# Kernel tuning notes

Measured on AMD Instinct MI355X. Metric: run time of the kernel, lower is better.

Reference implementation:

```python
import jax, jax.numpy as jnp
import numpy as np

B, C_IN, H, W = 4, 128, 32, 32
C_SKIP, C_OUT = 64, 64
D_MODEL = 2 * C_SKIP            # 128 (channels after concat)
D_STATE, D_CONV, EXPAND = 16, 4, 2
D_INNER = EXPAND * D_MODEL      # 256
DT_RANK = int(np.ceil(D_MODEL / 16))  # 8
LN_EPS = 1e-5


def setup_inputs() -> dict:
    key = jax.random.key(0)
    ks = jax.random.split(key, 12)
    s = 0.02
    return {
        "x": jax.random.normal(ks[0], (B, C_IN, H, W), jnp.float32),
        "skip_x": jax.random.normal(ks[1], (B, C_SKIP, 2 * H, 2 * W), jnp.float32),
        # ConvTranspose2d(in, skip, k=2, s=2): torch weight layout (in, out, kh, kw)
        "up_w": jax.random.normal(ks[2], (C_IN, C_SKIP, 2, 2), jnp.float32) * s,
        "up_b": jnp.zeros((C_SKIP,), jnp.float32),
        # Mamba params (torch Linear layout: (out_features, in_features))
        "in_proj_w": jax.random.normal(ks[3], (2 * D_INNER, D_MODEL), jnp.float32) * s,
        "conv1d_w": jax.random.normal(ks[4], (D_INNER, 1, D_CONV), jnp.float32) * s,
        "conv1d_b": jnp.zeros((D_INNER,), jnp.float32),
        "x_proj_w": jax.random.normal(ks[5], (DT_RANK + 2 * D_STATE, D_INNER), jnp.float32) * s,
        "dt_proj_w": jax.random.normal(ks[6], (D_INNER, DT_RANK), jnp.float32) * s,
        "dt_proj_b": jnp.zeros((D_INNER,), jnp.float32),
        "A_log": jnp.log(jnp.broadcast_to(jnp.arange(1, D_STATE + 1, dtype=jnp.float32), (D_INNER, D_STATE))),
        "Dp": jnp.ones((D_INNER,), jnp.float32),
        "out_proj_w": jax.random.normal(ks[7], (D_MODEL, D_INNER), jnp.float32) * s,
        "ln_gamma": jnp.ones((D_MODEL,), jnp.float32),
        "ln_beta": jnp.zeros((D_MODEL,), jnp.float32),
        # Conv2d 1x1 (out, in)
        "convout_w": jax.random.normal(ks[8], (C_OUT, D_MODEL), jnp.float32) * s,
        "convout_b": jnp.zeros((C_OUT,), jnp.float32),
    }


def _selective_scan(u, delta, A, Bm, Cm, Dp):
    # u, delta: (B,L,Din); A: (Din,Ds); Bm, Cm: (B,L,Ds)
    deltaA = jnp.exp(delta[..., None] * A)                        # (B,L,Din,Ds)
    deltaBu = delta[..., None] * Bm[:, :, None, :] * u[..., None]  # (B,L,Din,Ds)

    def step(h, xs):
        dA, dBu, c = xs                 # (B,Din,Ds),(B,Din,Ds),(B,Ds)
        h = dA * h + dBu
        y = jnp.einsum('bdn,bn->bd', h, c)
        return h, y

    h0 = jnp.zeros((u.shape[0], D_INNER, D_STATE), u.dtype)
    xs = (deltaA.transpose(1, 0, 2, 3), deltaBu.transpose(1, 0, 2, 3), Cm.transpose(1, 0, 2))
    _, ys = jax.lax.scan(step, h0, xs)  # (L,B,Din)
    return ys.transpose(1, 0, 2) + u * Dp


def _mamba(seq, in_proj_w, conv1d_w, conv1d_b, x_proj_w, dt_proj_w, dt_proj_b, A_log, Dp, out_proj_w):
    # seq: (B, L, D_MODEL)
    xz = seq @ in_proj_w.T                      # (B,L,2*Din)
    u, z = jnp.split(xz, 2, axis=-1)
    # depthwise causal conv1d along L
    uc = u.transpose(0, 2, 1)                   # (B,Din,L)
    uc = jax.lax.conv_general_dilated(
        uc, conv1d_w, window_strides=(1,), padding=[(D_CONV - 1, 0)],
        feature_group_count=D_INNER, dimension_numbers=('NCH', 'OIH', 'NCH'))
    uc = uc + conv1d_b[None, :, None]
    u = jax.nn.silu(uc.transpose(0, 2, 1))      # (B,L,Din)
    dbc = u @ x_proj_w.T                        # (B,L,DT_RANK+2*Ds)
    dt, Bm, Cm = jnp.split(dbc, [DT_RANK, DT_RANK + D_STATE], axis=-1)
    delta = jax.nn.softplus(dt @ dt_proj_w.T + dt_proj_b)
    A = -jnp.exp(A_log)
    y = _selective_scan(u, delta, A, Bm, Cm, Dp)
    y = y * jax.nn.silu(z)
    return y @ out_proj_w.T                     # (B,L,D_MODEL)


def reference(x, skip_x, up_w, up_b, in_proj_w, conv1d_w, conv1d_b, x_proj_w,
              dt_proj_w, dt_proj_b, A_log, Dp, out_proj_w, ln_gamma, ln_beta,
              convout_w, convout_b):
    b, _, h, w = x.shape
    # ConvTranspose2d k=2 s=2: each pixel expands to a 2x2 block
    up = jnp.einsum('bchw,coij->bohiwj', x, up_w).reshape(b, C_SKIP, 2 * h, 2 * w)
    up = up + up_b[None, :, None, None]
    xc = jnp.concatenate([up, skip_x], axis=1)  # (B, D_MODEL, 2H, 2W)
    Hh, Ww = xc.shape[2], xc.shape[3]
    seq = xc.reshape(b, D_MODEL, Hh * Ww).transpose(0, 2, 1)  # (B,L,D)
    y = _mamba(seq, in_proj_w, conv1d_w, conv1d_b, x_proj_w, dt_proj_w,
               dt_proj_b, A_log, Dp, out_proj_w)
    xm = y.transpose(0, 2, 1).reshape(b, D_MODEL, Hh, Ww)
    # permute -> LayerNorm over channels -> permute back
    xn = xm.transpose(0, 2, 3, 1)
    mu = xn.mean(-1, keepdims=True)
    var = xn.var(-1, keepdims=True)
    xn = (xn - mu) * jax.lax.rsqrt(var + LN_EPS) * ln_gamma + ln_beta
    xm = jax.nn.silu(xn.transpose(0, 3, 1, 2))
    out = jnp.einsum('bchw,oc->bohw', xm, convout_w) + convout_b[None, :, None, None]
    return out
```

## Files before the change

### kernel.cpp

```cpp
#include <hip/hip_runtime.h>

#define L_SEQ 4096
#define DM 128
#define DIN 256
#define NC 128
#define CHUNK 32

__global__ __launch_bounds__(256) void upcat_kernel(
    const float* __restrict__ x, const float* __restrict__ skip,
    const float* __restrict__ up_w, const float* __restrict__ up_b,
    float* __restrict__ seq) {
  int b = blockIdx.x >> 6, hh = blockIdx.x & 63;
  int h = hh >> 1, i = hh & 1;
  int tid = threadIdx.x;
  __shared__ float xs[128][32];
  __shared__ float wsh[2][128][64];
  for (int e = tid; e < 1024; e += 256) {
    int c = e >> 3, q = e & 7;
    *(float4*)&xs[c][q * 4] =
        *(const float4*)(x + (((size_t)b * 128 + c) * 32 + h) * 32 + q * 4);
  }
  for (int e = tid; e < 8192; e += 256) {
    int c = e >> 6, o = e & 63;
    float2 v = *(const float2*)(up_w + c * 256 + o * 4 + i * 2);
    wsh[0][c][o] = v.x;
    wsh[1][c][o] = v.y;
  }
  __syncthreads();
  int tx = tid & 15, ty = tid >> 4;
  float4 bv = *(const float4*)(up_b + tx * 4);
  float acc[4][4];
#pragma unroll
  for (int a = 0; a < 4; ++a) {
    acc[a][0] = bv.x; acc[a][1] = bv.y; acc[a][2] = bv.z; acc[a][3] = bv.w;
  }
#pragma unroll 4
  for (int c = 0; c < 128; ++c) {
    float x0 = xs[c][ty * 2];
    float x1 = xs[c][ty * 2 + 1];
    float4 w0 = *(const float4*)&wsh[0][c][tx * 4];
    float4 w1 = *(const float4*)&wsh[1][c][tx * 4];
    acc[0][0] = fmaf(x0, w0.x, acc[0][0]); acc[0][1] = fmaf(x0, w0.y, acc[0][1]);
    acc[0][2] = fmaf(x0, w0.z, acc[0][2]); acc[0][3] = fmaf(x0, w0.w, acc[0][3]);
    acc[1][0] = fmaf(x0, w1.x, acc[1][0]); acc[1][1] = fmaf(x0, w1.y, acc[1][1]);
    acc[1][2] = fmaf(x0, w1.z, acc[1][2]); acc[1][3] = fmaf(x0, w1.w, acc[1][3]);
    acc[2][0] = fmaf(x1, w0.x, acc[2][0]); acc[2][1] = fmaf(x1, w0.y, acc[2][1]);
    acc[2][2] = fmaf(x1, w0.z, acc[2][2]); acc[2][3] = fmaf(x1, w0.w, acc[2][3]);
    acc[3][0] = fmaf(x1, w1.x, acc[3][0]); acc[3][1] = fmaf(x1, w1.y, acc[3][1]);
    acc[3][2] = fmaf(x1, w1.z, acc[3][2]); acc[3][3] = fmaf(x1, w1.w, acc[3][3]);
  }
  size_t mrow_base = (size_t)b * L_SEQ + (size_t)hh * 64;
#pragma unroll
  for (int a = 0; a < 4; ++a) {
    int ww = ty * 4 + a;
    *(float4*)(seq + (mrow_base + ww) * DM + tx * 4) =
        make_float4(acc[a][0], acc[a][1], acc[a][2], acc[a][3]);
  }
  for (int e = tid; e < 4096; e += 256) {
    int c = e & 63, ww = e >> 6;
    seq[(mrow_base + ww) * DM + 64 + c] =
        skip[((size_t)b * 64 + c) * (size_t)L_SEQ + hh * 64 + ww];
  }
}

__global__ __launch_bounds__(256) void gemm_bt128(
    const float* __restrict__ A, const float* __restrict__ W,
    float* __restrict__ C, int M, int N, int K) {
  __shared__ float As[32][132];
  __shared__ float Ws[32][68];
  int m0 = blockIdx.x * 128, n0 = blockIdx.y * 64;
  int tid = threadIdx.x;
  int tx = tid & 15, ty = tid >> 4;
  float acc[8][4];
#pragma unroll
  for (int a = 0; a < 8; ++a)
#pragma unroll
    for (int bb = 0; bb < 4; ++bb) acc[a][bb] = 0.f;

  for (int k0 = 0; k0 < K; k0 += 32) {
    __syncthreads();
    for (int e = tid; e < 1024; e += 256) {
      int r = e >> 3, c4 = (e & 7) << 2;
      float4 va = *(const float4*)(A + (size_t)(m0 + r) * K + k0 + c4);
      As[c4 + 0][r] = va.x; As[c4 + 1][r] = va.y;
      As[c4 + 2][r] = va.z; As[c4 + 3][r] = va.w;
    }
    for (int e = tid; e < 512; e += 256) {
      int r = e >> 3, c4 = (e & 7) << 2;
      float4 vw = *(const float4*)(W + (size_t)(n0 + r) * K + k0 + c4);
      Ws[c4 + 0][r] = vw.x; Ws[c4 + 1][r] = vw.y;
      Ws[c4 + 2][r] = vw.z; Ws[c4 + 3][r] = vw.w;
    }
    __syncthreads();
#pragma unroll
    for (int kk = 0; kk < 32; ++kk) {
      float4 a0 = *(const float4*)(&As[kk][ty * 8]);
      float4 a1 = *(const float4*)(&As[kk][ty * 8 + 4]);
      float4 wv = *(const float4*)(&Ws[kk][tx * 4]);
      float a_[8] = {a0.x, a0.y, a0.z, a0.w, a1.x, a1.y, a1.z, a1.w};
      float w_[4] = {wv.x, wv.y, wv.z, wv.w};
#pragma unroll
      for (int a = 0; a < 8; ++a)
#pragma unroll
        for (int bb = 0; bb < 4; ++bb)
          acc[a][bb] = fmaf(a_[a], w_[bb], acc[a][bb]);
    }
  }
#pragma unroll
  for (int a = 0; a < 8; ++a)
#pragma unroll
    for (int bb = 0; bb < 4; ++bb)
      C[(size_t)(m0 + ty * 8 + a) * N + n0 + tx * 4 + bb] = acc[a][bb];
}

__global__ __launch_bounds__(256) void gemm_bt(
    const float* __restrict__ A, const float* __restrict__ W,
    float* __restrict__ C, int M, int N, int K) {
  __shared__ float As[32][68];
  __shared__ float Ws[32][68];
  int m0 = blockIdx.x * 64, n0 = blockIdx.y * 64;
  int tid = threadIdx.x;
  int tx = tid & 15, ty = tid >> 4;
  float acc[4][4];
#pragma unroll
  for (int a = 0; a < 4; ++a)
#pragma unroll
    for (int bb = 0; bb < 4; ++bb) acc[a][bb] = 0.f;

  for (int k0 = 0; k0 < K; k0 += 32) {
    __syncthreads();
    for (int e = tid; e < 512; e += 256) {
      int r = e >> 3;
      int c4 = (e & 7) << 2;
      float4 va = *(const float4*)(A + (size_t)(m0 + r) * K + k0 + c4);
      As[c4 + 0][r] = va.x; As[c4 + 1][r] = va.y;
      As[c4 + 2][r] = va.z; As[c4 + 3][r] = va.w;
      float4 vw = *(const float4*)(W + (size_t)(n0 + r) * K + k0 + c4);
      Ws[c4 + 0][r] = vw.x; Ws[c4 + 1][r] = vw.y;
      Ws[c4 + 2][r] = vw.z; Ws[c4 + 3][r] = vw.w;
    }
    __syncthreads();
#pragma unroll
    for (int kk = 0; kk < 32; ++kk) {
      float4 av = *(const float4*)(&As[kk][ty * 4]);
      float4 wv = *(const float4*)(&Ws[kk][tx * 4]);
      float av_[4] = {av.x, av.y, av.z, av.w};
      float wv_[4] = {wv.x, wv.y, wv.z, wv.w};
#pragma unroll
      for (int a = 0; a < 4; ++a)
#pragma unroll
        for (int bb = 0; bb < 4; ++bb)
          acc[a][bb] = fmaf(av_[a], wv_[bb], acc[a][bb]);
    }
  }
#pragma unroll
  for (int a = 0; a < 4; ++a)
#pragma unroll
    for (int bb = 0; bb < 4; ++bb)
      C[(size_t)(m0 + ty * 4 + a) * N + n0 + tx * 4 + bb] = acc[a][bb];
}

__global__ __launch_bounds__(256) void xproj_kernel(
    const float* __restrict__ xz, const float* __restrict__ cw,
    const float* __restrict__ cb, const float* __restrict__ W,
    float* __restrict__ dbc, float* __restrict__ u_out) {
  __shared__ float xzt[67][64];
  __shared__ float us[64][68];
  int m0 = blockIdx.x * 64;
  int tid = threadIdx.x;
  int lane = tid & 63;
  int w = __builtin_amdgcn_readfirstlane(tid >> 6);
  int jbase = blockIdx.y * 20 + w * 5;
  const float* Wb = W + jbase * 256;
  bool first = (m0 & (L_SEQ - 1)) == 0;
  int cc4 = (tid & 15) << 2;
  int r0 = tid >> 4;
  float acc[5];
#pragma unroll
  for (int j = 0; j < 5; ++j) acc[j] = 0.f;
  for (int k0 = 0; k0 < 256; k0 += 64) {
    __syncthreads();
    for (int e = tid; e < 67 * 16; e += 256) {
      int rr = e >> 4, c4 = (e & 15) << 2;
      float4 v;
      if (first && rr < 3)
        v = make_float4(0.f, 0.f, 0.f, 0.f);
      else
        v = *(const float4*)(xz + (size_t)(m0 - 3 + rr) * 512 + k0 + c4);
      *(float4*)&xzt[rr][c4] = v;
    }
    __syncthreads();
    {
      int d = k0 + cc4;
      float4 cw0 = *(const float4*)(cw + (d + 0) * 4);
      float4 cw1 = *(const float4*)(cw + (d + 1) * 4);
      float4 cw2 = *(const float4*)(cw + (d + 2) * 4);
      float4 cw3 = *(const float4*)(cw + (d + 3) * 4);
      float4 cbv = *(const float4*)(cb + d);
#pragma unroll
      for (int s = 0; s < 4; ++s) {
        int r = r0 + s * 16;
        float a0 = cbv.x, a1 = cbv.y, a2 = cbv.z, a3 = cbv.w;
        a0 = fmaf(xzt[r + 0][cc4 + 0], cw0.x, a0);
        a0 = fmaf(xzt[r + 1][cc4 + 0], cw0.y, a0);
        a0 = fmaf(xzt[r + 2][cc4 + 0], cw0.z, a0);
        a0 = fmaf(xzt[r + 3][cc4 + 0], cw0.w, a0);
        a1 = fmaf(xzt[r + 0][cc4 + 1], cw1.x, a1);
        a1 = fmaf(xzt[r + 1][cc4 + 1], cw1.y, a1);
        a1 = fmaf(xzt[r + 2][cc4 + 1], cw1.z, a1);
        a1 = fmaf(xzt[r + 3][cc4 + 1], cw1.w, a1);
        a2 = fmaf(xzt[r + 0][cc4 + 2], cw2.x, a2);
        a2 = fmaf(xzt[r + 1][cc4 + 2], cw2.y, a2);
        a2 = fmaf(xzt[r + 2][cc4 + 2], cw2.z, a2);
        a2 = fmaf(xzt[r + 3][cc4 + 2], cw2.w, a2);
        a3 = fmaf(xzt[r + 0][cc4 + 3], cw3.x, a3);
        a3 = fmaf(xzt[r + 1][cc4 + 3], cw3.y, a3);
        a3 = fmaf(xzt[r + 2][cc4 + 3], cw3.z, a3);
        a3 = fmaf(xzt[r + 3][cc4 + 3], cw3.w, a3);
        float o0 = a0 / (1.f + __expf(-a0));
        float o1 = a1 / (1.f + __expf(-a1));
        float o2 = a2 / (1.f + __expf(-a2));
        float o3 = a3 / (1.f + __expf(-a3));
        *(float4*)&us[r][cc4] = make_float4(o0, o1, o2, o3);
        if (blockIdx.y == 0)
          *(float4*)(u_out + (size_t)(m0 + r) * 256 + d) =
              make_float4(o0, o1, o2, o3);
      }
    }
    __syncthreads();
#pragma unroll
    for (int kk = 0; kk < 64; kk += 4) {
      float4 a4 = *(const float4*)&us[lane][kk];
      float a_[4] = {a4.x, a4.y, a4.z, a4.w};
#pragma unroll
      for (int i = 0; i < 4; ++i)
#pragma unroll
        for (int j = 0; j < 5; ++j)
          acc[j] = fmaf(a_[i], Wb[j * 256 + k0 + kk + i], acc[j]);
    }
  }
  size_t base = (size_t)(m0 + lane) * 40 + jbase;
#pragma unroll
  for (int j = 0; j < 5; ++j) dbc[base + j] = acc[j];
}

__device__ __forceinline__ float softplus_f(float a) {
  return (a > 20.f) ? a : log1pf(__expf(a));
}

__global__ __launch_bounds__(256) void scan_pass1(
    const float* __restrict__ u, const float* __restrict__ dbc,
    const float* __restrict__ A_log, const float* __restrict__ Wdt,
    const float* __restrict__ bdt, float* __restrict__ carryA,
    float* __restrict__ carryH) {
  int bid = blockIdx.x;
  int b = bid >> 7;
  int c = bid & (NC - 1);
  int d = threadIdx.x;
  __shared__ float ls[CHUNK * 40];
  size_t l0 = (size_t)b * L_SEQ + (size_t)c * CHUNK;
  const float* rp = dbc + l0 * 40;
  for (int e = d; e < CHUNK * 40; e += 256) ls[e] = rp[e];
  float Ac[16];
  {
    const float4* ar = (const float4*)(A_log + d * 16);
#pragma unroll
    for (int q = 0; q < 4; ++q) {
      float4 v = ar[q];
      Ac[q * 4 + 0] = -__expf(v.x); Ac[q * 4 + 1] = -__expf(v.y);
      Ac[q * 4 + 2] = -__expf(v.z); Ac[q * 4 + 3] = -__expf(v.w);
    }
  }
  float wdt[8];
  {
    const float4* wr = (const float4*)(Wdt + d * 8);
    float4 v0 = wr[0], v1 = wr[1];
    wdt[0] = v0.x; wdt[1] = v0.y; wdt[2] = v0.z; wdt[3] = v0.w;
    wdt[4] = v1.x; wdt[5] = v1.y; wdt[6] = v1.z; wdt[7] = v1.w;
  }
  float bdt_v = bdt[d];
  const float* up = u + l0 * 256 + d;
  __syncthreads();
  float h[16];
#pragma unroll
  for (int n = 0; n < 16; ++n) h[n] = 0.f;
  float dvs = 0.f;
#pragma unroll 4
  for (int li = 0; li < CHUNK; ++li) {
    float uv = up[(size_t)li * 256];
    float acc = bdt_v;
#pragma unroll
    for (int j = 0; j < 8; ++j)
      acc = fmaf(ls[li * 40 + j], wdt[j], acc);
    float dv = softplus_f(acc);
    dvs += dv;
    float t = dv * uv;
#pragma unroll
    for (int n = 0; n < 16; ++n) {
      float dA = __expf(dv * Ac[n]);
      h[n] = fmaf(dA, h[n], t * ls[li * 40 + 8 + n]);
    }
  }
  float4* cA = (float4*)(carryA + ((size_t)bid * 256 + d) * 16);
  float4* cH = (float4*)(carryH + ((size_t)bid * 256 + d) * 16);
#pragma unroll
  for (int q = 0; q < 4; ++q) {
    cA[q] = make_float4(__expf(dvs * Ac[q * 4]), __expf(dvs * Ac[q * 4 + 1]),
                        __expf(dvs * Ac[q * 4 + 2]), __expf(dvs * Ac[q * 4 + 3]));
    cH[q] = make_float4(h[q * 4], h[q * 4 + 1], h[q * 4 + 2], h[q * 4 + 3]);
  }
}

__global__ __launch_bounds__(256) void scan_mid(
    const float* __restrict__ carryA, float* __restrict__ carryH) {
  int gid = blockIdx.x * 256 + threadIdx.x;
  int b = gid >> 12;
  int dn = gid & 4095;
  float h = 0.f;
  for (int c = 0; c < NC; ++c) {
    size_t i = ((size_t)(b * NC + c) << 12) + dn;
    float a = carryA[i];
    float hl = carryH[i];
    carryH[i] = h;
    h = fmaf(a, h, hl);
  }
}

__global__ __launch_bounds__(256) void scan_pass3(
    const float* __restrict__ u, const float* __restrict__ dbc,
    const float* __restrict__ xz, const float* __restrict__ A_log,
    const float* __restrict__ Wdt, const float* __restrict__ bdt,
    const float* __restrict__ Dp, const float* __restrict__ carryH,
    float* __restrict__ y) {
  int bid = blockIdx.x;
  int b = bid >> 7;
  int c = bid & (NC - 1);
  int d = threadIdx.x;
  __shared__ float ls[CHUNK * 40];
  size_t l0 = (size_t)b * L_SEQ + (size_t)c * CHUNK;
  const float* rp = dbc + l0 * 40;
  for (int e = d; e < CHUNK * 40; e += 256) ls[e] = rp[e];
  float Ac[16];
  {
    const float4* ar = (const float4*)(A_log + d * 16);
#pragma unroll
    for (int q = 0; q < 4; ++q) {
      float4 v = ar[q];
      Ac[q * 4 + 0] = -__expf(v.x); Ac[q * 4 + 1] = -__expf(v.y);
      Ac[q * 4 + 2] = -__expf(v.z); Ac[q * 4 + 3] = -__expf(v.w);
    }
  }
  float wdt[8];
  {
    const float4* wr = (const float4*)(Wdt + d * 8);
    float4 v0 = wr[0], v1 = wr[1];
    wdt[0] = v0.x; wdt[1] = v0.y; wdt[2] = v0.z; wdt[3] = v0.w;
    wdt[4] = v1.x; wdt[5] = v1.y; wdt[6] = v1.z; wdt[7] = v1.w;
  }
  float bdt_v = bdt[d];
  float Dv = Dp[d];
  float h[16];
  {
    const float4* cH = (const float4*)(carryH + ((size_t)bid * 256 + d) * 16);
#pragma unroll
    for (int q = 0; q < 4; ++q) {
      float4 v = cH[q];
      h[q * 4 + 0] = v.x; h[q * 4 + 1] = v.y;
      h[q * 4 + 2] = v.z; h[q * 4 + 3] = v.w;
    }
  }
  const float* up = u + l0 * 256 + d;
  const float* zp = xz + l0 * 512 + 256 + d;
  float* yp = y + l0 * 256 + d;
  __syncthreads();
#pragma unroll 4
  for (int li = 0; li < CHUNK; ++li) {
    float uv = up[(size_t)li * 256];
    float zv = zp[(size_t)li * 512];
    float acc = bdt_v;
#pragma unroll
    for (int j = 0; j < 8; ++j)
      acc = fmaf(ls[li * 40 + j], wdt[j], acc);
    float dv = softplus_f(acc);
    float t = dv * uv;
    float p = 0.f;
#pragma unroll
    for (int n = 0; n < 16; ++n) {
      float dA = __expf(dv * Ac[n]);
      h[n] = fmaf(dA, h[n], t * ls[li * 40 + 8 + n]);
      p = fmaf(h[n], ls[li * 40 + 24 + n], p);
    }
    float s = zv / (1.f + __expf(-zv));
    yp[(size_t)li * 256] = (p + uv * Dv) * s;
  }
}

__global__ __launch_bounds__(256) void ln_out_kernel(
    const float* __restrict__ s2, const float* __restrict__ gamma,
    const float* __restrict__ beta, const float* __restrict__ Wo,
    const float* __restrict__ bo, float* __restrict__ out) {
  __shared__ float xt[64][129];
  __shared__ float mus[64], invs[64];
  int tid = threadIdx.x;
  int m0 = blockIdx.x * 64;
  for (int i = 0; i < 8; ++i) {
    int s = tid + i * 256;
    int r = s >> 5, q = s & 31;
    float4 v = *(const float4*)(s2 + (size_t)(m0 + r) * 128 + q * 4);
    xt[r][q * 4 + 0] = v.x; xt[r][q * 4 + 1] = v.y;
    xt[r][q * 4 + 2] = v.z; xt[r][q * 4 + 3] = v.w;
  }
  __syncthreads();
  {
    int r = tid >> 2, kq = (tid & 3) * 32;
    float s = 0.f, q = 0.f;
#pragma unroll 8
    for (int kk = 0; kk < 32; ++kk) {
      float v = xt[r][kq + kk];
      s += v; q = fmaf(v, v, q);
    }
    s += __shfl_xor(s, 1, 64); s += __shfl_xor(s, 2, 64);
    q += __shfl_xor(q, 1, 64); q += __shfl_xor(q, 2, 64);
    if ((tid & 3) == 0) {
      float mu = s * (1.f / 128.f);
      float var = q * (1.f / 128.f) - mu * mu;
      mus[r] = mu;
      invs[r] = rsqrtf(var + 1e-5f);
    }
  }
  __syncthreads();
  for (int i = 0; i < 32; ++i) {
    int idx = tid + i * 256;
    int r = idx >> 7, k = idx & 127;
    float v = xt[r][k];
    float xn = (v - mus[r]) * invs[r] * gamma[k] + beta[k];
    xt[r][k] = xn / (1.f + __expf(-xn));
  }
  __syncthreads();
  int lane = tid & 63;
  int w = __builtin_amdgcn_readfirstlane(tid >> 6);
  int cbase = blockIdx.y * 32 + w * 8;
  const float* Wrow = Wo + cbase * 128;
  float acc[8];
#pragma unroll
  for (int j = 0; j < 8; ++j) acc[j] = 0.f;
#pragma unroll 4
  for (int k = 0; k < 128; ++k) {
    float v = xt[lane][k];
#pragma unroll
    for (int j = 0; j < 8; ++j)
      acc[j] = fmaf(v, Wrow[j * 128 + k], acc[j]);
  }
  int m = m0 + lane;
  int b = m >> 12, l = m & 4095;
#pragma unroll
  for (int j = 0; j < 8; ++j)
    out[((size_t)b * 64 + cbase + j) * 4096 + l] = acc[j] + bo[cbase + j];
}

extern "C" void kernel_launch(void* const* d_in, const int* in_sizes, int n_in,
                              void* d_out, int out_size, void* d_ws, size_t ws_size,
                              hipStream_t stream) {
  (void)in_sizes; (void)n_in; (void)out_size; (void)ws_size;
  const float* x         = (const float*)d_in[0];
  const float* skip      = (const float*)d_in[1];
  const float* up_w      = (const float*)d_in[2];
  const float* up_b      = (const float*)d_in[3];
  const float* in_proj_w = (const float*)d_in[4];
  const float* conv1d_w  = (const float*)d_in[5];
  const float* conv1d_b  = (const float*)d_in[6];
  const float* x_proj_w  = (const float*)d_in[7];
  const float* dt_proj_w = (const float*)d_in[8];
  const float* dt_proj_b = (const float*)d_in[9];
  const float* A_log     = (const float*)d_in[10];
  const float* Dp        = (const float*)d_in[11];
  const float* out_proj_w= (const float*)d_in[12];
  const float* ln_gamma  = (const float*)d_in[13];
  const float* ln_beta   = (const float*)d_in[14];
  const float* convout_w = (const float*)d_in[15];
  const float* convout_b = (const float*)d_in[16];
  float* out = (float*)d_out;
  float* ws  = (float*)d_ws;

  float* seq    = ws;
  float* xz     = ws + 2097152;
  float* u      = ws + 10485760;
  float* dbc    = ws + 14680064;
  float* y      = ws + 15335424;
  float* carryA = ws + 19529728;
  float* carryH = ws + 21626880;

  upcat_kernel<<<256, 256, 0, stream>>>(x, skip, up_w, up_b, seq);
  gemm_bt128<<<dim3(16384 / 128, 512 / 64), 256, 0, stream>>>(
      seq, in_proj_w, xz, 16384, 512, 128);
  xproj_kernel<<<dim3(16384 / 64, 2), 256, 0, stream>>>(
      xz, conv1d_w, conv1d_b, x_proj_w, dbc, u);
  scan_pass1<<<4 * NC, 256, 0, stream>>>(u, dbc, A_log, dt_proj_w, dt_proj_b,
                                         carryA, carryH);
  scan_mid<<<64, 256, 0, stream>>>(carryA, carryH);
  scan_pass3<<<4 * NC, 256, 0, stream>>>(u, dbc, xz, A_log, dt_proj_w,
                                         dt_proj_b, Dp, carryH, y);
  gemm_bt<<<dim3(16384 / 64, 128 / 64), 256, 0, stream>>>(y, out_proj_w, seq,
                                                          16384, 128, 256);
  ln_out_kernel<<<dim3(256, 2), 256, 0, stream>>>(seq, ln_gamma, ln_beta,
                                                  convout_w, convout_b, out);
}
```

Measured before the change: 193.5 us.

## Fuse out_proj GEMM with LayerNorm and output conv; spread scan_mid over more blocks

The out_proj GEMM now runs in the same kernel as LayerNorm, SiLU and the 1x1 output conv. Each block computes a full 64x128 row tile into shared memory and then applies the rest, so the intermediate buffer no longer makes a round trip through global memory and one launch is removed. The cost is that each block now does all 64 output channels, which means fewer blocks (256 instead of 512) and more shared memory, so occupancy drops. scan_mid is relaunched as 256 blocks of 64 threads and prefetches the next chunk's carries to hide load latency in the serial loop.

```diff
diff --git a/kernel.cpp b/kernel.cpp
--- a/kernel.cpp
+++ b/kernel.cpp
@@ -111,53 +111,6 @@
 #pragma unroll
     for (int bb = 0; bb < 4; ++bb)
       C[(size_t)(m0 + ty * 8 + a) * N + n0 + tx * 4 + bb] = acc[a][bb];
-}
-
-__global__ __launch_bounds__(256) void gemm_bt(
-    const float* __restrict__ A, const float* __restrict__ W,
-    float* __restrict__ C, int M, int N, int K) {
-  __shared__ float As[32][68];
-  __shared__ float Ws[32][68];
-  int m0 = blockIdx.x * 64, n0 = blockIdx.y * 64;
-  int tid = threadIdx.x;
-  int tx = tid & 15, ty = tid >> 4;
-  float acc[4][4];
-#pragma unroll
-  for (int a = 0; a < 4; ++a)
-#pragma unroll
-    for (int bb = 0; bb < 4; ++bb) acc[a][bb] = 0.f;
-
-  for (int k0 = 0; k0 < K; k0 += 32) {
-    __syncthreads();
-    for (int e = tid; e < 512; e += 256) {
-      int r = e >> 3;
-      int c4 = (e & 7) << 2;
-      float4 va = *(const float4*)(A + (size_t)(m0 + r) * K + k0 + c4);
-      As[c4 + 0][r] = va.x; As[c4 + 1][r] = va.y;
-      As[c4 + 2][r] = va.z; As[c4 + 3][r] = va.w;
-      float4 vw = *(const float4*)(W + (size_t)(n0 + r) * K + k0 + c4);
-      Ws[c4 + 0][r] = vw.x; Ws[c4 + 1][r] = vw.y;
-      Ws[c4 + 2][r] = vw.z; Ws[c4 + 3][r] = vw.w;
-    }
-    __syncthreads();
-#pragma unroll
-    for (int kk = 0; kk < 32; ++kk) {
-      float4 av = *(const float4*)(&As[kk][ty * 4]);
-      float4 wv = *(const float4*)(&Ws[kk][tx * 4]);
-      float av_[4] = {av.x, av.y, av.z, av.w};
-      float wv_[4] = {wv.x, wv.y, wv.z, wv.w};
-#pragma unroll
-      for (int a = 0; a < 4; ++a)
-#pragma unroll
-        for (int bb = 0; bb < 4; ++bb)
-          acc[a][bb] = fmaf(av_[a], wv_[bb], acc[a][bb]);
-    }
-  }
-#pragma unroll
-  for (int a = 0; a < 4; ++a)
-#pragma unroll
-    for (int bb = 0; bb < 4; ++bb)
-      C[(size_t)(m0 + ty * 4 + a) * N + n0 + tx * 4 + bb] = acc[a][bb];
 }
 
 __global__ __launch_bounds__(256) void xproj_kernel(
@@ -311,19 +264,24 @@
   }
 }
 
-__global__ __launch_bounds__(256) void scan_mid(
+__global__ __launch_bounds__(64) void scan_mid(
     const float* __restrict__ carryA, float* __restrict__ carryH) {
-  int gid = blockIdx.x * 256 + threadIdx.x;
+  int gid = blockIdx.x * 64 + threadIdx.x;
   int b = gid >> 12;
   int dn = gid & 4095;
+  size_t i = ((size_t)(b * NC) << 12) + dn;
   float h = 0.f;
-  for (int c = 0; c < NC; ++c) {
-    size_t i = ((size_t)(b * NC + c) << 12) + dn;
-    float a = carryA[i];
-    float hl = carryH[i];
+  float a = carryA[i], hl = carryH[i];
+#pragma unroll 4
+  for (int c = 0; c < NC - 1; ++c) {
+    size_t i2 = i + 4096;
+    float a2 = carryA[i2];
+    float hl2 = carryH[i2];
     carryH[i] = h;
     h = fmaf(a, h, hl);
-  }
+    a = a2; hl = hl2; i = i2;
+  }
+  carryH[i] = h;
 }
 
 __global__ __launch_bounds__(256) void scan_pass3(
@@ -395,21 +353,59 @@
   }
 }
 
-__global__ __launch_bounds__(256) void ln_out_kernel(
-    const float* __restrict__ s2, const float* __restrict__ gamma,
-    const float* __restrict__ beta, const float* __restrict__ Wo,
-    const float* __restrict__ bo, float* __restrict__ out) {
+__global__ __launch_bounds__(256) void fused_out_kernel(
+    const float* __restrict__ y, const float* __restrict__ Wp,
+    const float* __restrict__ gamma, const float* __restrict__ beta,
+    const float* __restrict__ Wo, const float* __restrict__ bo,
+    float* __restrict__ out) {
+  __shared__ float As[32][68];
+  __shared__ float Ws[32][132];
   __shared__ float xt[64][129];
   __shared__ float mus[64], invs[64];
   int tid = threadIdx.x;
   int m0 = blockIdx.x * 64;
-  for (int i = 0; i < 8; ++i) {
-    int s = tid + i * 256;
-    int r = s >> 5, q = s & 31;
-    float4 v = *(const float4*)(s2 + (size_t)(m0 + r) * 128 + q * 4);
-    xt[r][q * 4 + 0] = v.x; xt[r][q * 4 + 1] = v.y;
-    xt[r][q * 4 + 2] = v.z; xt[r][q * 4 + 3] = v.w;
-  }
+  int tx = tid & 15, ty = tid >> 4;
+  float acc[4][8];
+#pragma unroll
+  for (int a = 0; a < 4; ++a)
+#pragma unroll
+    for (int bb = 0; bb < 8; ++bb) acc[a][bb] = 0.f;
+
+  for (int k0 = 0; k0 < 256; k0 += 32) {
+    __syncthreads();
+    for (int e = tid; e < 512; e += 256) {
+      int r = e >> 3, c4 = (e & 7) << 2;
+      float4 va = *(const float4*)(y + (size_t)(m0 + r) * 256 + k0 + c4);
+      As[c4 + 0][r] = va.x; As[c4 + 1][r] = va.y;
+      As[c4 + 2][r] = va.z; As[c4 + 3][r] = va.w;
+    }
+    for (int e = tid; e < 1024; e += 256) {
+      int n = e >> 3, c4 = (e & 7) << 2;
+      float4 vw = *(const float4*)(Wp + (size_t)n * 256 + k0 + c4);
+      Ws[c4 + 0][n] = vw.x; Ws[c4 + 1][n] = vw.y;
+      Ws[c4 + 2][n] = vw.z; Ws[c4 + 3][n] = vw.w;
+    }
+    __syncthreads();
+#pragma unroll
+    for (int kk = 0; kk < 32; ++kk) {
+      float4 av = *(const float4*)(&As[kk][ty * 4]);
+      float4 w0 = *(const float4*)(&Ws[kk][tx * 8]);
+      float4 w1 = *(const float4*)(&Ws[kk][tx * 8 + 4]);
+      float a_[4] = {av.x, av.y, av.z, av.w};
+      float w_[8] = {w0.x, w0.y, w0.z, w0.w, w1.x, w1.y, w1.z, w1.w};
+#pragma unroll
+      for (int a = 0; a < 4; ++a)
+#pragma unroll
+        for (int bb = 0; bb < 8; ++bb)
+          acc[a][bb] = fmaf(a_[a], w_[bb], acc[a][bb]);
+    }
+  }
+  __syncthreads();
+#pragma unroll
+  for (int a = 0; a < 4; ++a)
+#pragma unroll
+    for (int bb = 0; bb < 8; ++bb)
+      xt[ty * 4 + a][tx * 8 + bb] = acc[a][bb];
   __syncthreads();
   {
     int r = tid >> 2, kq = (tid & 3) * 32;
@@ -439,23 +435,23 @@
   __syncthreads();
   int lane = tid & 63;
   int w = __builtin_amdgcn_readfirstlane(tid >> 6);
-  int cbase = blockIdx.y * 32 + w * 8;
+  int cbase = w * 16;
   const float* Wrow = Wo + cbase * 128;
-  float acc[8];
-#pragma unroll
-  for (int j = 0; j < 8; ++j) acc[j] = 0.f;
+  float acc2[16];
+#pragma unroll
+  for (int j = 0; j < 16; ++j) acc2[j] = 0.f;
 #pragma unroll 4
   for (int k = 0; k < 128; ++k) {
     float v = xt[lane][k];
 #pragma unroll
-    for (int j = 0; j < 8; ++j)
-      acc[j] = fmaf(v, Wrow[j * 128 + k], acc[j]);
+    for (int j = 0; j < 16; ++j)
+      acc2[j] = fmaf(v, Wrow[j * 128 + k], acc2[j]);
   }
   int m = m0 + lane;
   int b = m >> 12, l = m & 4095;
 #pragma unroll
-  for (int j = 0; j < 8; ++j)
-    out[((size_t)b * 64 + cbase + j) * 4096 + l] = acc[j] + bo[cbase + j];
+  for (int j = 0; j < 16; ++j)
+    out[((size_t)b * 64 + cbase + j) * 4096 + l] = acc2[j] + bo[cbase + j];
 }
 
 extern "C" void kernel_launch(void* const* d_in, const int* in_sizes, int n_in,
@@ -497,11 +493,9 @@
       xz, conv1d_w, conv1d_b, x_proj_w, dbc, u);
   scan_pass1<<<4 * NC, 256, 0, stream>>>(u, dbc, A_log, dt_proj_w, dt_proj_b,
                                          carryA, carryH);
-  scan_mid<<<64, 256, 0, stream>>>(carryA, carryH);
+  scan_mid<<<256, 64, 0, stream>>>(carryA, carryH);
   scan_pass3<<<4 * NC, 256, 0, stream>>>(u, dbc, xz, A_log, dt_proj_w,
                                          dt_proj_b, Dp, carryH, y);
-  gemm_bt<<<dim3(16384 / 64, 128 / 64), 256, 0, stream>>>(y, out_proj_w, seq,
-                                                          16384, 128, 256);
-  ln_out_kernel<<<dim3(256, 2), 256, 0, stream>>>(seq, ln_gamma, ln_beta,
-                                                  convout_w, convout_b, out);
-}
+  fused_out_kernel<<<256, 256, 0, stream>>>(y, out_proj_w, ln_gamma, ln_beta,
+                                            convout_w, convout_b, out);
+}
```

Result: slower. 214.3 us (+10.7%).
